# Kernel optimization log

Measured on AMD Instinct MI355X. Metric: run time of the kernel, lower is better.

The kernel has to match this reference:

```python
import jax, jax.numpy as jnp
import numpy as np


def _lstm_dir(x, w_ih, w_hh, b, reverse):
    # x: [S,B,I], w_ih: [4H,I], w_hh: [4H,H], b: [4H]. torch gate order i,f,g,o.
    H = w_hh.shape[1]
    gx = jnp.einsum('sbi,gi->sbg', x, w_ih) + b  # precompute input projections
    B = x.shape[1]
    h0 = jnp.zeros((B, H), x.dtype)

    def step(carry, g):
        h, c = carry
        z = g + h @ w_hh.T
        i, f, gg, o = jnp.split(z, 4, axis=-1)
        c = jax.nn.sigmoid(f) * c + jax.nn.sigmoid(i) * jnp.tanh(gg)
        h = jax.nn.sigmoid(o) * jnp.tanh(c)
        return (h, c), h

    (hT, _), hs = jax.lax.scan(step, (h0, h0), gx, reverse=reverse)
    return hs, hT  # hs: [S,B,H] in original time order; hT final hidden


def _bilstm_layer(x, w_ih, w_hh, b):
    # x: [S,B,I]; params stacked [2, ...] for (forward, backward)
    hs_f, hT_f = _lstm_dir(x, w_ih[0], w_hh[0], b[0], reverse=False)
    hs_b, hT_b = _lstm_dir(x, w_ih[1], w_hh[1], b[1], reverse=True)
    return jnp.concatenate([hs_f, hs_b], axis=-1), hT_f, hT_b


def reference(tokens, emb, w_ih0, w_hh0, b0, w_ih1, w_hh1, b1, fc1_w, fc1_b, fc2_w, fc2_b):
    # tokens: [B,S] int; embedding lookup (frozen table)
    x = emb[tokens]                       # [B,S,E]
    x = jnp.transpose(x, (1, 0, 2))       # [S,B,E] time-major for scan
    h0_seq, _, _ = _bilstm_layer(x, w_ih0, w_hh0, b0)          # [S,B,2H]
    _, hT_f, hT_b = _bilstm_layer(h0_seq, w_ih1, w_hh1, b1)    # final layer
    out = jnp.concatenate([hT_f, hT_b], axis=-1)               # [B,2H]
    out = jax.nn.relu(out @ fc1_w.T + fc1_b)
    return out @ fc2_w.T + fc2_b          # [B,2]


def setup_inputs() -> dict:
    key = jax.random.key(0)
    ks = jax.random.split(key, 13)
    B, S, V, E, H = 256, 512, 50000, 300, 128
    s = 0.05
    return {
        'tokens': jax.random.randint(ks[0], (B, S), 0, V, dtype=jnp.int32),
        'emb':    jax.random.normal(ks[1], (V, E), jnp.float32) * s,
        'w_ih0':  jax.random.normal(ks[2], (2, 4 * H, E), jnp.float32) * s,
        'w_hh0':  jax.random.normal(ks[3], (2, 4 * H, H), jnp.float32) * s,
        'b0':     jax.random.normal(ks[4], (2, 4 * H), jnp.float32) * s,
        'w_ih1':  jax.random.normal(ks[5], (2, 4 * H, 2 * H), jnp.float32) * s,
        'w_hh1':  jax.random.normal(ks[6], (2, 4 * H, H), jnp.float32) * s,
        'b1':     jax.random.normal(ks[7], (2, 4 * H), jnp.float32) * s,
        'fc1_w':  jax.random.normal(ks[8], (H, 2 * H), jnp.float32) * s,
        'fc1_b':  jax.random.normal(ks[9], (H,), jnp.float32) * s,
        'fc2_w':  jax.random.normal(ks[10], (2, H), jnp.float32) * s,
        'fc2_b':  jax.random.normal(ks[11], (2,), jnp.float32) * s,
    }
```

## Files before the change

kernel.cpp:

```cpp
#include <hip/hip_runtime.h>

#define S_LEN 512
#define BATCH 256
#define EMB_D 300
#define EMB_PAD 320
#define HID 128
#define SB (S_LEN*BATCH)
#define CH 128
#define NCH 4
#define GXC_DIR ((size_t)CH*BATCH*512)
#define SMEM_BYTES 86016

typedef __attribute__((ext_vector_type(8))) short bf16x8;
typedef __attribute__((ext_vector_type(4))) float f32x4;
typedef unsigned short u16;
typedef unsigned int   u32;

__device__ __forceinline__ float b2f(u16 u) {
    union { u32 i; float f; } v; v.i = ((u32)u) << 16; return v.f;
}
__device__ __forceinline__ u16 f2b(float f) {
    union { float f; u32 i; } v; v.f = f;
    u32 r = v.i + 0x7fffu + ((v.i >> 16) & 1u);
    return (u16)(r >> 16);
}
__device__ __forceinline__ float sigf(float x) {
    return __builtin_amdgcn_rcpf(1.f + __expf(-x));
}
__device__ __forceinline__ float tanhf_fast(float x) {
    float e = __expf(2.f * x);
    return 1.f - 2.f * __builtin_amdgcn_rcpf(e + 1.f);
}

__global__ void k_detect(const u16* __restrict__ emb_u, int* __restrict__ flag) {
    __shared__ int cnt;
    if (threadIdx.x == 0) cnt = 0;
    __syncthreads();
    float v = b2f(emb_u[2 * threadIdx.x + 64]);
    float a = fabsf(v);
    if (a > 1e-4f && a < 16.f) atomicAdd(&cnt, 1);
    __syncthreads();
    if (threadIdx.x == 0) *flag = (cnt > 128) ? 1 : 0;
}

__global__ void k_packw(const void* __restrict__ src, u16* __restrict__ dst,
                        int Kin, int Kpad, int total, const int* __restrict__ flag) {
    int i = blockIdx.x * 256 + threadIdx.x;
    if (i >= total) return;
    int n = i / Kpad, k = i - n * Kpad;
    int d = n >> 9, r = n & 511, j = r >> 2, t = r & 3;
    size_t si = (size_t)((d << 9) + (t << 7) + j) * Kin + k;
    u16 v = 0;
    if (k < Kin) {
        if (*flag) v = ((const u16*)src)[si];
        else       v = f2b(((const float*)src)[si]);
    }
    dst[i] = v;
}

__global__ void k_packb(const void* __restrict__ src, float* __restrict__ dst,
                        const int* __restrict__ flag) {
    int i = blockIdx.x * 256 + threadIdx.x;
    if (i >= 1024) return;
    int d = i >> 9, r = i & 511, j = r >> 2, t = r & 3;
    size_t si = (d << 9) + (t << 7) + j;
    dst[i] = (*flag) ? b2f(((const u16*)src)[si]) : ((const float*)src)[si];
}

template<int KPAD, bool EMBED, bool IS_L0>
__global__ __launch_bounds__(1024) void k_fused(
    const int* __restrict__ tok, const void* __restrict__ Asrc,
    const u16* __restrict__ W, const float* __restrict__ bias,
    u16* __restrict__ gx_out, const u16* __restrict__ gx_in,
    const u16* __restrict__ Whp,
    u16* __restrict__ h0seq, float* __restrict__ hT,
    u16* __restrict__ hstate, float* __restrict__ cstate,
    int k, int nlstm, int soff0g, int soff1g, const int* __restrict__ flag)
{
    __shared__ __align__(16) char smem[SMEM_BYTES];
    const int tid = threadIdx.x;

    if ((int)blockIdx.x < nlstm) {
        u16* hb = (u16*)smem;
        u16* gb = (u16*)(smem + 8704);
        const int d    = blockIdx.x >> 4;
        const int bg   = blockIdx.x & 15;
        const int wv   = tid >> 6, lane = tid & 63, quad = lane >> 4, col = lane & 15;
        const int soff = (d == 0) ? CH * k : CH * (NCH - 1 - k);

        for (int i = tid; i < 2 * 16 * 136; i += 1024) hb[i] = 0;
        __syncthreads();
        if (k > 0) {
            for (int i = tid; i < 16 * 128; i += 1024) {
                int bl = i >> 7, j = i & 127;
                hb[bl * 136 + j] = hstate[((size_t)d * BATCH + bg * 16 + bl) * 128 + j];
            }
        }

        const u16* Wd = Whp + (size_t)d * 512 * 128;
        bf16x8 wf[2][4];
#pragma unroll
        for (int mt = 0; mt < 2; ++mt)
#pragma unroll
            for (int ks = 0; ks < 4; ++ks)
                wf[mt][ks] = *(const bf16x8*)(Wd + (size_t)(((wv * 2 + mt) * 16) + col) * 128 + ks * 32 + quad * 8);

        const u16* gxd = gx_in + (size_t)d * GXC_DIR;
        auto sloc = [&](int si) { return (d == 0) ? si : (CH - 1 - si); };
        auto prefetch = [&](int si, int P) {
            const u16* g0 = gxd + ((size_t)sloc(si) * BATCH + bg * 16 + wv) * 512 + lane * 8;
            __builtin_amdgcn_global_load_lds((const __attribute__((address_space(1))) void*)g0,
                (__attribute__((address_space(3))) void*)(gb + (P * 16 + wv) * 520), 16, 0, 0);
        };

        float c[2];
#pragma unroll
        for (int mt = 0; mt < 2; ++mt)
            c[mt] = (k > 0) ? cstate[((size_t)d * BATCH + bg * 16 + col) * 128 + (wv * 2 + mt) * 4 + quad] : 0.f;

        auto step = [&](int si, int P) {
            if (si + 1 < CH) prefetch(si + 1, P ^ 1);
            if constexpr (IS_L0) {
                if (si > 0) {
                    int sp = soff + ((d == 0) ? (si - 1) : (CH - si));
                    ushort2 hv = *(const ushort2*)(hb + (P * 16 + wv) * 136 + lane * 2);
                    *(ushort2*)(h0seq + ((size_t)sp * BATCH + bg * 16 + wv) * 256 + (d << 7) + lane * 2) = hv;
                }
            }
            bf16x8 hf[4];
#pragma unroll
            for (int ks = 0; ks < 4; ++ks)
                hf[ks] = *(const bf16x8*)(hb + (P * 16 + col) * 136 + ks * 32 + quad * 8);
            f32x4 z[2];
#pragma unroll
            for (int mt = 0; mt < 2; ++mt) {
                ushort4 gv = *(const ushort4*)(gb + (P * 16 + col) * 520 + (wv * 2 + mt) * 16 + quad * 4);
                z[mt][0] = b2f(gv.x); z[mt][1] = b2f(gv.y); z[mt][2] = b2f(gv.z); z[mt][3] = b2f(gv.w);
            }
#pragma unroll
            for (int ks = 0; ks < 4; ++ks)
#pragma unroll
                for (int mt = 0; mt < 2; ++mt)
                    z[mt] = __builtin_amdgcn_mfma_f32_16x16x32_bf16(wf[mt][ks], hf[ks], z[mt], 0, 0, 0);
#pragma unroll
            for (int mt = 0; mt < 2; ++mt) {
                float iv = sigf(z[mt][0]), fv = sigf(z[mt][1]);
                float gg = tanhf_fast(z[mt][2]), ov = sigf(z[mt][3]);
                c[mt] = fv * c[mt] + iv * gg;
                float hv = ov * tanhf_fast(c[mt]);
                const int j = (wv * 2 + mt) * 4 + quad;
                hb[((P ^ 1) * 16 + col) * 136 + j] = f2b(hv);
                if constexpr (!IS_L0) {
                    if (k == NCH - 1 && si == CH - 1)
                        hT[((size_t)d * BATCH + bg * 16 + col) * 128 + j] = hv;
                }
            }
            __syncthreads();
        };

        prefetch(0, 0);
        __syncthreads();

        for (int si = 0; si < CH; si += 2) {
            step(si, 0);
            step(si + 1, 1);
        }

        if constexpr (IS_L0) {
            int sp = soff + ((d == 0) ? (CH - 1) : 0);
            ushort2 hv = *(const ushort2*)(hb + wv * 136 + lane * 2);
            *(ushort2*)(h0seq + ((size_t)sp * BATCH + bg * 16 + wv) * 256 + (d << 7) + lane * 2) = hv;
        }
        if (k < NCH - 1) {
            for (int i = tid; i < 16 * 128; i += 1024) {
                int bl = i >> 7, j = i & 127;
                hstate[((size_t)d * BATCH + bg * 16 + bl) * 128 + j] = hb[bl * 136 + j];
            }
#pragma unroll
            for (int mt = 0; mt < 2; ++mt)
                cstate[((size_t)d * BATCH + bg * 16 + col) * 128 + (wv * 2 + mt) * 4 + quad] = c[mt];
        }
        return;
    }

    const int g = (int)blockIdx.x - nlstm;
    constexpr int KSTEPS = KPAD / 32;
    constexpr int AST    = KPAD + 8;
    constexpr int NCHK   = 64 * (KPAD / 8);
    u16* As = (u16*)smem;
    u16* Bs = (u16*)(smem + (size_t)64 * AST * 2);
    const int dir  = g >> 9;
    const int m0   = (g & 511) * 64;
    const int soff = dir ? soff1g : soff0g;
    const size_t mg0 = (size_t)soff * BATCH;
    const int w = tid >> 6, lane = tid & 63, quad = lane >> 4, l16 = lane & 15;
    const int wm = w >> 2, wn = w & 3;
    const bool is_bf = EMBED ? (*flag != 0) : true;

    for (int ch = tid; ch < NCHK; ch += 1024) {
        int row = ch / (KPAD / 8), seg = ch % (KPAD / 8);
        uint4 v;
        if constexpr (EMBED) {
            u32 u[4];
            size_t m = mg0 + m0 + row;
            int s = (int)(m >> 8), b = (int)(m & 255);
            size_t aro = (size_t)tok[b * S_LEN + s] * EMB_D;
            if (is_bf) {
                const u16* ar = (const u16*)Asrc + aro;
#pragma unroll
                for (int i = 0; i < 4; ++i) {
                    int cc = seg * 8 + 2 * i;
                    u[i] = (cc < EMB_D) ? *(const u32*)(ar + cc) : 0u;
                }
            } else {
                const float* ar = (const float*)Asrc + aro;
#pragma unroll
                for (int i = 0; i < 4; ++i) {
                    int cc = seg * 8 + 2 * i;
                    if (cc < EMB_D) {
                        float2 f = *(const float2*)(ar + cc);
                        u[i] = (u32)f2b(f.x) | ((u32)f2b(f.y) << 16);
                    } else u[i] = 0u;
                }
            }
            v.x = u[0]; v.y = u[1]; v.z = u[2]; v.w = u[3];
        } else {
            v = *(const uint4*)((const u16*)Asrc + (mg0 + m0 + row) * KPAD + seg * 8);
        }
        *(uint4*)(As + (size_t)row * AST + seg * 8) = v;
    }

    for (int j = 0; j < 8; ++j) {
        __syncthreads();
        for (int ch = tid; ch < NCHK; ch += 1024) {
            int row = ch / (KPAD / 8), seg = ch % (KPAD / 8);
            uint4 v = *(const uint4*)(W + (size_t)(dir * 512 + j * 64 + row) * KPAD + seg * 8);
            *(uint4*)(Bs + (size_t)row * AST + seg * 8) = v;
        }
        __syncthreads();
        f32x4 acc = {};
#pragma unroll
        for (int kk = 0; kk < KSTEPS; ++kk) {
            bf16x8 af = *(const bf16x8*)(As + (size_t)(wm * 16 + l16) * AST + kk * 32 + quad * 8);
            bf16x8 bf = *(const bf16x8*)(Bs + (size_t)(wn * 16 + l16) * AST + kk * 32 + quad * 8);
            acc = __builtin_amdgcn_mfma_f32_16x16x32_bf16(af, bf, acc, 0, 0, 0);
        }
#pragma unroll
        for (int r = 0; r < 4; ++r) {
            int mloc = m0 + wm * 16 + quad * 4 + r;
            int nloc = j * 64 + wn * 16 + l16;
            float vv = acc[r] + bias[dir * 512 + nloc];
            gx_out[(size_t)dir * GXC_DIR + (size_t)mloc * 512 + nloc] = f2b(vv);
        }
    }
}

__global__ void k_fc(const float* __restrict__ hT,
                     const void* __restrict__ fc1w, const void* __restrict__ fc1b,
                     const void* __restrict__ fc2w, const void* __restrict__ fc2b,
                     void* __restrict__ out, const int* __restrict__ flag) {
    int b = blockIdx.x, j = threadIdx.x;
    bool is_bf = (*flag != 0);
    __shared__ float u[128];
    float a = is_bf ? b2f(((const u16*)fc1b)[j]) : ((const float*)fc1b)[j];
    for (int k = 0; k < 256; ++k) {
        float x = hT[((size_t)(k >> 7) * BATCH + b) * 128 + (k & 127)];
        float w = is_bf ? b2f(((const u16*)fc1w)[j * 256 + k]) : ((const float*)fc1w)[j * 256 + k];
        a += x * w;
    }
    u[j] = fmaxf(a, 0.f);
    __syncthreads();
    if (j < 2) {
        float a2 = is_bf ? b2f(((const u16*)fc2b)[j]) : ((const float*)fc2b)[j];
        for (int q = 0; q < 128; ++q) {
            float w = is_bf ? b2f(((const u16*)fc2w)[j * 128 + q]) : ((const float*)fc2w)[j * 128 + q];
            a2 += u[q] * w;
        }
        if (is_bf) ((u16*)out)[b * 2 + j] = f2b(a2);
        else       ((float*)out)[b * 2 + j] = a2;
    }
}

extern "C" void kernel_launch(void* const* d_in, const int* in_sizes, int n_in,
                              void* d_out, int out_size, void* d_ws, size_t ws_size,
                              hipStream_t stream) {
    const int*  tok   = (const int*)d_in[0];
    const void* emb   = d_in[1];
    const void* w_ih0 = d_in[2];
    const void* w_hh0 = d_in[3];
    const void* b0    = d_in[4];
    const void* w_ih1 = d_in[5];
    const void* w_hh1 = d_in[6];
    const void* b1    = d_in[7];
    const void* fc1w  = d_in[8];
    const void* fc1b  = d_in[9];
    const void* fc2w  = d_in[10];
    const void* fc2b  = d_in[11];

    char* ws = (char*)d_ws;
    size_t off = 0;
    auto alloc = [&](size_t bytes) -> void* {
        void* p = ws + off; off += (bytes + 255) & ~(size_t)255; return p;
    };
    int*   flag   = (int*)alloc(256);
    u16*   Wp0    = (u16*)alloc(1024 * 320 * 2);
    u16*   Wp1    = (u16*)alloc(1024 * 256 * 2);
    u16*   Whp0   = (u16*)alloc(1024 * 128 * 2);
    u16*   Whp1   = (u16*)alloc(1024 * 128 * 2);
    float* bp0    = (float*)alloc(1024 * 4);
    float* bp1    = (float*)alloc(1024 * 4);
    float* hT     = (float*)alloc((size_t)2 * BATCH * 128 * 4);
    u16*   hstate = (u16*)alloc((size_t)2 * BATCH * 128 * 2);
    float* cstate = (float*)alloc((size_t)2 * BATCH * 128 * 4);
    u16*   h0seq  = (u16*)alloc((size_t)SB * 256 * 2);
    size_t bufb   = 2 * GXC_DIR * sizeof(u16);
    u16*   gxcA   = (u16*)alloc(bufb);
    bool overlap  = ws_size >= off + bufb;
    u16*   gxcB   = overlap ? (u16*)alloc(bufb) : gxcA;

    k_detect<<<1, 256, 0, stream>>>((const u16*)emb, flag);

    k_packw<<<(1024 * 320 + 255) / 256, 256, 0, stream>>>(w_ih0, Wp0, 300, 320, 1024 * 320, flag);
    k_packw<<<(1024 * 256 + 255) / 256, 256, 0, stream>>>(w_ih1, Wp1, 256, 256, 1024 * 256, flag);
    k_packw<<<(1024 * 128 + 255) / 256, 256, 0, stream>>>(w_hh0, Whp0, 128, 128, 1024 * 128, flag);
    k_packw<<<(1024 * 128 + 255) / 256, 256, 0, stream>>>(w_hh1, Whp1, 128, 128, 1024 * 128, flag);
    k_packb<<<4, 256, 0, stream>>>(b0, bp0, flag);
    k_packb<<<4, 256, 0, stream>>>(b1, bp1, flag);

    const int NG = 1024;

    if (overlap) {
        k_fused<320, true, true><<<NG, 1024, 0, stream>>>(
            tok, emb, Wp0, bp0, gxcA, gxcA, Whp0, h0seq, nullptr, hstate, cstate,
            0, 0, 0, CH * (NCH - 1), flag);
        for (int k = 0; k < NCH; ++k) {
            int ng = (k < NCH - 1) ? NG : 0;
            u16* gin  = (k & 1) ? gxcB : gxcA;
            u16* gout = (k & 1) ? gxcA : gxcB;
            k_fused<320, true, true><<<32 + ng, 1024, 0, stream>>>(
                tok, emb, Wp0, bp0, gout, gin, Whp0, h0seq, nullptr, hstate, cstate,
                k, 32, CH * (k + 1), CH * (NCH - 2 - k), flag);
        }
        k_fused<256, false, false><<<NG, 1024, 0, stream>>>(
            nullptr, h0seq, Wp1, bp1, gxcA, gxcA, Whp1, nullptr, hT, hstate, cstate,
            0, 0, 0, CH * (NCH - 1), flag);
        for (int k = 0; k < NCH; ++k) {
            int ng = (k < NCH - 1) ? NG : 0;
            u16* gin  = (k & 1) ? gxcB : gxcA;
            u16* gout = (k & 1) ? gxcA : gxcB;
            k_fused<256, false, false><<<32 + ng, 1024, 0, stream>>>(
                nullptr, h0seq, Wp1, bp1, gout, gin, Whp1, nullptr, hT, hstate, cstate,
                k, 32, CH * (k + 1), CH * (NCH - 2 - k), flag);
        }
    } else {
        for (int k = 0; k < NCH; ++k) {
            k_fused<320, true, true><<<NG, 1024, 0, stream>>>(
                tok, emb, Wp0, bp0, gxcA, gxcA, Whp0, h0seq, nullptr, hstate, cstate,
                0, 0, CH * k, CH * (NCH - 1 - k), flag);
            k_fused<320, true, true><<<32, 1024, 0, stream>>>(
                tok, emb, Wp0, bp0, gxcA, gxcA, Whp0, h0seq, nullptr, hstate, cstate,
                k, 32, 0, 0, flag);
        }
        for (int k = 0; k < NCH; ++k) {
            k_fused<256, false, false><<<NG, 1024, 0, stream>>>(
                nullptr, h0seq, Wp1, bp1, gxcA, gxcA, Whp1, nullptr, hT, hstate, cstate,
                0, 0, CH * k, CH * (NCH - 1 - k), flag);
            k_fused<256, false, false><<<32, 1024, 0, stream>>>(
                nullptr, h0seq, Wp1, bp1, gxcA, gxcA, Whp1, nullptr, hT, hstate, cstate,
                k, 32, 0, 0, flag);
        }
    }
    k_fc<<<256, 128, 0, stream>>>(hT, fc1w, fc1b, fc2w, fc2b, d_out, flag);
}
```

Baseline: 1.568 ms.

## Double-buffer weight tiles and cache A fragments in registers for input-projection GEMM

The input-projection GEMM blocks now prefetch the next 64-row weight tile into registers while running MFMAs on the current tile, then write it to a second shared-memory buffer. This leaves one barrier per iteration instead of two and overlaps global weight loads with compute. The A-operand fragments are loaded from shared memory once into registers and reused across all eight N-tiles. In exchange, shared memory per block grows (86 KB to 126 KB) and register pressure rises, which may lower occupancy, and the LSTM blocks sharing the launch may be affected by the larger dynamic smem size.

```diff
diff --git a/kernel.cpp b/kernel.cpp
--- a/kernel.cpp
+++ b/kernel.cpp
@@ -9,7 +9,7 @@
 #define CH 128
 #define NCH 4
 #define GXC_DIR ((size_t)CH*BATCH*512)
-#define SMEM_BYTES 86016
+#define SMEM_BYTES 125952
 
 typedef __attribute__((ext_vector_type(8))) short bf16x8;
 typedef __attribute__((ext_vector_type(4))) float f32x4;
@@ -186,9 +186,11 @@
     const int g = (int)blockIdx.x - nlstm;
     constexpr int KSTEPS = KPAD / 32;
     constexpr int AST    = KPAD + 8;
-    constexpr int NCHK   = 64 * (KPAD / 8);
-    u16* As = (u16*)smem;
-    u16* Bs = (u16*)(smem + (size_t)64 * AST * 2);
+    constexpr int CPR    = KPAD / 8;
+    constexpr int NCHK   = 64 * CPR;
+    u16* As  = (u16*)smem;
+    u16* Bs0 = (u16*)(smem + (size_t)64 * AST * 2);
+    u16* Bs1 = Bs0 + (size_t)64 * AST;
     const int dir  = g >> 9;
     const int m0   = (g & 511) * 64;
     const int soff = dir ? soff1g : soff0g;
@@ -196,9 +198,10 @@
     const int w = tid >> 6, lane = tid & 63, quad = lane >> 4, l16 = lane & 15;
     const int wm = w >> 2, wn = w & 3;
     const bool is_bf = EMBED ? (*flag != 0) : true;
+    const u16* Wdir = W + (size_t)dir * 512 * KPAD;
 
     for (int ch = tid; ch < NCHK; ch += 1024) {
-        int row = ch / (KPAD / 8), seg = ch % (KPAD / 8);
+        int row = ch / CPR, seg = ch % CPR;
         uint4 v;
         if constexpr (EMBED) {
             u32 u[4];
@@ -229,22 +232,47 @@
         }
         *(uint4*)(As + (size_t)row * AST + seg * 8) = v;
     }
+    for (int ch = tid; ch < NCHK; ch += 1024) {
+        int row = ch / CPR, seg = ch % CPR;
+        uint4 v = *(const uint4*)(Wdir + (size_t)row * KPAD + seg * 8);
+        *(uint4*)(Bs0 + (size_t)row * AST + seg * 8) = v;
+    }
+    __syncthreads();
+
+    bf16x8 afr[KSTEPS];
+#pragma unroll
+    for (int kk = 0; kk < KSTEPS; ++kk)
+        afr[kk] = *(const bf16x8*)(As + (size_t)(wm * 16 + l16) * AST + kk * 32 + quad * 8);
 
     for (int j = 0; j < 8; ++j) {
+        uint4 v0, v1, v2;
+        const bool more = (j + 1 < 8);
+        if (more) {
+            const u16* Wj = Wdir + (size_t)(j + 1) * 64 * KPAD;
+            { int row = tid / CPR, seg = tid % CPR;
+              v0 = *(const uint4*)(Wj + (size_t)row * KPAD + seg * 8); }
+            { int ch = tid + 1024; int row = ch / CPR, seg = ch % CPR;
+              v1 = *(const uint4*)(Wj + (size_t)row * KPAD + seg * 8); }
+            if (tid + 2048 < NCHK) { int ch = tid + 2048; int row = ch / CPR, seg = ch % CPR;
+              v2 = *(const uint4*)(Wj + (size_t)row * KPAD + seg * 8); }
+        }
+        const u16* Bc = (j & 1) ? Bs1 : Bs0;
+        f32x4 acc = {};
+#pragma unroll
+        for (int kk = 0; kk < KSTEPS; ++kk) {
+            bf16x8 bf = *(const bf16x8*)(Bc + (size_t)(wn * 16 + l16) * AST + kk * 32 + quad * 8);
+            acc = __builtin_amdgcn_mfma_f32_16x16x32_bf16(afr[kk], bf, acc, 0, 0, 0);
+        }
+        if (more) {
+            u16* Bn = (j & 1) ? Bs0 : Bs1;
+            { int row = tid / CPR, seg = tid % CPR;
+              *(uint4*)(Bn + (size_t)row * AST + seg * 8) = v0; }
+            { int ch = tid + 1024; int row = ch / CPR, seg = ch % CPR;
+              *(uint4*)(Bn + (size_t)row * AST + seg * 8) = v1; }
+            if (tid + 2048 < NCHK) { int ch = tid + 2048; int row = ch / CPR, seg = ch % CPR;
+              *(uint4*)(Bn + (size_t)row * AST + seg * 8) = v2; }
+        }
         __syncthreads();
-        for (int ch = tid; ch < NCHK; ch += 1024) {
-            int row = ch / (KPAD / 8), seg = ch % (KPAD / 8);
-            uint4 v = *(const uint4*)(W + (size_t)(dir * 512 + j * 64 + row) * KPAD + seg * 8);
-            *(uint4*)(Bs + (size_t)row * AST + seg * 8) = v;
-        }
-        __syncthreads();
-        f32x4 acc = {};
-#pragma unroll
-        for (int kk = 0; kk < KSTEPS; ++kk) {
-            bf16x8 af = *(const bf16x8*)(As + (size_t)(wm * 16 + l16) * AST + kk * 32 + quad * 8);
-            bf16x8 bf = *(const bf16x8*)(Bs + (size_t)(wn * 16 + l16) * AST + kk * 32 + quad * 8);
-            acc = __builtin_amdgcn_mfma_f32_16x16x32_bf16(af, bf, acc, 0, 0, 0);
-        }
 #pragma unroll
         for (int r = 0; r < 4; ++r) {
             int mloc = m0 + wm * 16 + quad * 4 + r;
```

Result: faster. 1.527 ms (-2.6%).
